# Performance work log

Hardware: AMD Instinct MI355X
Metric: run time of the kernel (lower is better)

Reference implementation:

```python
import jax, jax.numpy as jnp
import numpy as np

N = 2          # batch (upsample scale for sample i is i+1, shapes chosen so no crop occurs)
C = 512        # channels for both branches
TH = TW = 256  # target H,W taken from pts_feats[0]
IMG_SIZES = [128, 64, 32, 16, 8]  # 5-level FPN
BN_EPS = 1e-5


def setup_inputs() -> dict:
    key = jax.random.key(0)
    ks = jax.random.split(key, 24)
    inp = {}
    for l, s in enumerate(IMG_SIZES):
        inp[f'img_feat{l}'] = jax.random.normal(ks[l], (N, C, s, s), jnp.float32)
    inp['pts_feat0'] = jax.random.normal(ks[5], (N, C, TH, TW), jnp.float32)
    # 1x1 conv + BN params (eval-mode BN with running stats)
    inp['img_w'] = jax.random.normal(ks[6], (C, C), jnp.float32) * 0.02
    inp['img_b'] = jax.random.normal(ks[7], (C,), jnp.float32) * 0.02
    inp['img_gamma'] = jnp.ones((C,), jnp.float32)
    inp['img_beta'] = jnp.zeros((C,), jnp.float32)
    inp['img_mean'] = jnp.zeros((C,), jnp.float32)
    inp['img_var'] = jax.random.uniform(ks[8], (C,), jnp.float32, 0.5, 1.5)
    inp['pts_w'] = jax.random.normal(ks[9], (C, C), jnp.float32) * 0.02
    inp['pts_b'] = jax.random.normal(ks[10], (C,), jnp.float32) * 0.02
    inp['pts_gamma'] = jnp.ones((C,), jnp.float32)
    inp['pts_beta'] = jnp.zeros((C,), jnp.float32)
    inp['pts_mean'] = jnp.zeros((C,), jnp.float32)
    inp['pts_var'] = jax.random.uniform(ks[11], (C,), jnp.float32, 0.5, 1.5)
    return inp


def _obtain_mlvl(feats, th, tw):
    # Faithful to original: per-sample loop (scale_factor depends on batch index,
    # so each sample has a different static upsampled shape -> Python loop over N=2).
    n = feats[0].shape[0]
    outs = []
    for i in range(n):
        acc = None
        for lvl, f in enumerate(feats):
            x = f[i]  # [C, h, w]
            if lvl > 0:
                s = i + 1  # nearest upsample by batch-index+1 (as in source)
                x = jnp.repeat(jnp.repeat(x, s, axis=1), s, axis=2)
            dh = th - x.shape[1]
            dw = tw - x.shape[2]
            x = jnp.pad(x, ((0, 0), (dh // 2, dh - dh // 2), (dw // 2, dw - dw // 2)), mode='edge')
            acc = x if acc is None else acc + x
        outs.append(acc)
    return jnp.stack(outs, 0)  # [N, C, th, tw]


def _conv_bn_relu(x, w, b, gamma, beta, mean, var):
    # 1x1 conv == channel contraction, then eval-mode BN, then ReLU
    y = jnp.einsum('nchw,oc->nohw', x, w) + b[None, :, None, None]
    scale = gamma / jnp.sqrt(var + BN_EPS)
    y = (y - mean[None, :, None, None]) * scale[None, :, None, None] + beta[None, :, None, None]
    return jax.nn.relu(y)


def reference(img_feat0, img_feat1, img_feat2, img_feat3, img_feat4, pts_feat0,
              img_w, img_b, img_gamma, img_beta, img_mean, img_var,
              pts_w, pts_b, pts_gamma, pts_beta, pts_mean, pts_var):
    th, tw = pts_feat0.shape[2], pts_feat0.shape[3]
    pts_m = _obtain_mlvl([pts_feat0], th, tw)  # pts_levels=1
    pts_pre = _conv_bn_relu(pts_m, pts_w, pts_b, pts_gamma, pts_beta, pts_mean, pts_var)
    img_m = _obtain_mlvl([img_feat0, img_feat1, img_feat2, img_feat3, img_feat4], th, tw)
    img_pre = _conv_bn_relu(img_m, img_w, img_b, img_gamma, img_beta, img_mean, img_var)
    # dropout is identity in eval mode (deterministic reference)
    return jnp.concatenate((img_pre, pts_pre), axis=1)  # [N, 2C, th, tw]
```

## Files before the change

### kernel.cpp

```cpp
#include <hip/hip_runtime.h>

typedef unsigned short u16;
typedef __attribute__((ext_vector_type(8))) short s8frag;
typedef __attribute__((ext_vector_type(4))) float f32x4;

#define GLOAD16(gp, lp)                                                        \
  __builtin_amdgcn_global_load_lds(                                            \
      (const __attribute__((address_space(1))) void*)(gp),                     \
      (__attribute__((address_space(3))) void*)(lp), 16, 0, 0)

__device__ __forceinline__ u16 f2bf(float x) {
  unsigned int u = __float_as_uint(x);
  unsigned int r = (u + 0x7fffu + ((u >> 16) & 1u)) >> 16;
  return (u16)r;
}

__global__ __launch_bounds__(256) void prep_w(
    const float* __restrict__ wi, const float* __restrict__ bi,
    const float* __restrict__ gi, const float* __restrict__ bei,
    const float* __restrict__ mi, const float* __restrict__ vi,
    const float* __restrict__ wp, const float* __restrict__ bp,
    const float* __restrict__ gp, const float* __restrict__ bep,
    const float* __restrict__ mp, const float* __restrict__ vp,
    u16* __restrict__ wout_i, float* __restrict__ bias_i,
    u16* __restrict__ wout_p, float* __restrict__ bias_p) {
  int gidx = blockIdx.x * 256 + threadIdx.x;
  int branch = gidx >> 18;
  int idx = gidx & ((1 << 18) - 1);
  int o = idx >> 9, c = idx & 511;
  const float* w = branch ? wp : wi;
  const float* b = branch ? bp : bi;
  const float* g = branch ? gp : gi;
  const float* be = branch ? bep : bei;
  const float* mn = branch ? mp : mi;
  const float* vr = branch ? vp : vi;
  u16* wo = branch ? wout_p : wout_i;
  float* bo = branch ? bias_p : bias_i;
  float scale = g[o] * rsqrtf(vr[o] + 1e-5f);
  wo[idx] = f2bf(w[idx] * scale);
  if (c == 0) bo[o] = scale * (b[o] - mn[o]) + be[o];
}

__global__ __launch_bounds__(256) void build_b(
    const float* __restrict__ f0, const float* __restrict__ f1,
    const float* __restrict__ f2, const float* __restrict__ f3,
    const float* __restrict__ f4, const float* __restrict__ pts,
    u16* __restrict__ Bimg, u16* __restrict__ Bpts) {
  __shared__ float tile[64][65];
  int t = threadIdx.x;
  int wblk = blockIdx.x;
  int h = blockIdx.y;
  int z = blockIdx.z;
  bool is_img = z < 16;
  int zz = is_img ? z : z - 16;
  int n = zz >> 3;
  int cblk = zz & 7;
  int cbase = cblk * 64;

  if (is_img) {
    int wl = t & 63, w = wblk * 64 + wl;
    const float* feats[5] = {f0, f1, f2, f3, f4};
    const int S[5] = {128, 64, 32, 16, 8};
    int off[5];
#pragma unroll
    for (int l = 0; l < 5; ++l) {
      int s = S[l];
      int scale = (n == 1 && l > 0) ? 2 : 1;
      int u = s * scale, pad = (256 - u) >> 1;
      int ih = h - pad; ih = ih < 0 ? 0 : (ih > u - 1 ? u - 1 : ih); ih /= scale;
      int iw = w - pad; iw = iw < 0 ? 0 : (iw > u - 1 ? u - 1 : iw); iw /= scale;
      off[l] = ih * s + iw;
    }
    for (int cs = 0; cs < 16; ++cs) {
      int cl = cs * 4 + (t >> 6);
      int c = cbase + cl;
      float acc = 0.f;
#pragma unroll
      for (int l = 0; l < 5; ++l) {
        int s = S[l];
        acc += feats[l][(long)(n * 512 + c) * s * s + off[l]];
      }
      tile[cl][wl] = acc;
    }
  } else {
    int wq = t & 15;
    int cl0 = t >> 4;
#pragma unroll
    for (int j = 0; j < 4; ++j) {
      int cl = cl0 + j * 16;
      int c = cbase + cl;
      float4 v = *(const float4*)&pts[((long)(n * 512 + c) * 256 + h) * 256 +
                                      wblk * 64 + wq * 4];
      tile[cl][wq * 4 + 0] = v.x;
      tile[cl][wq * 4 + 1] = v.y;
      tile[cl][wq * 4 + 2] = v.z;
      tile[cl][wq * 4 + 3] = v.w;
    }
  }
  __syncthreads();

  u16* dst = is_img ? Bimg : Bpts;
  long hwb = (long)h * 256 + wblk * 64;
#pragma unroll
  for (int half = 0; half < 2; ++half) {
    int c0 = (t & 7) * 8;
    int wl2 = half * 32 + (t >> 3);
    u16 p[8];
#pragma unroll
    for (int j = 0; j < 8; ++j) p[j] = f2bf(tile[c0 + j][wl2]);
    long di = ((long)n * 65536 + hwb + wl2) * 512 + cbase + c0;
    *(uint4*)(dst + di) = *(const uint4*)p;
  }
}

__global__ __launch_bounds__(256, 2) void gemm_fused(
    const u16* __restrict__ Aimg, const u16* __restrict__ Apts,
    const u16* __restrict__ Bimg, const u16* __restrict__ Bpts,
    const float* __restrict__ biasImg, const float* __restrict__ biasPts,
    float* __restrict__ out) {
  int br = blockIdx.z;
  const u16* A = br ? Apts : Aimg;
  const u16* B = br ? Bpts : Bimg;
  const float* bias = br ? biasPts : biasImg;

  int s = blockIdx.x;
  int w = (s & 7) * 512 + (s >> 3);
  int rt = w & 3;
  int ct = w >> 2;
  int n = ct >> 9;
  int colbase = (ct & 511) * 128;
  const u16* Bn = B + ((long)n * 65536) * 512;

  __shared__ u16 As[2][128 * 64];
  __shared__ u16 Bs[2][128 * 64];

  int t = threadIdx.x;
  int wave = t >> 6, lane = t & 63;
  int wr = wave >> 1, wc = wave & 1;
  int lrow = lane & 15;
  int q = lane >> 4;

  f32x4 acc[4][4] = {};

#define STAGE_A(buf, kt_)                                                     \
  {                                                                           \
    int kk_ = (kt_) * 64;                                                     \
    _Pragma("unroll") for (int i = 0; i < 4; ++i) {                           \
      int slot = t + i * 256;                                                 \
      int row = slot >> 3, kp = slot & 7;                                     \
      GLOAD16(A + ((long)(rt * 128 + row) * 512 + kk_ + ((kp ^ (row & 7)) * 8)), \
              &As[buf][slot * 8]);                                            \
    }                                                                         \
  }
#define STAGE_B(buf, kt_)                                                     \
  {                                                                           \
    int kk_ = (kt_) * 64;                                                     \
    _Pragma("unroll") for (int i = 0; i < 4; ++i) {                           \
      int slot = t + i * 256;                                                 \
      int row = slot >> 3, kp = slot & 7;                                     \
      GLOAD16(Bn + ((long)(colbase + row) * 512 + kk_ + ((kp ^ (row & 7)) * 8)), \
              &Bs[buf][slot * 8]);                                            \
    }                                                                         \
  }

  STAGE_A(0, 0);
  STAGE_B(0, 0);
  asm volatile("s_waitcnt vmcnt(0)" ::: "memory");
  __builtin_amdgcn_s_barrier();

#pragma unroll 1
  for (int kt = 0; kt < 8; ++kt) {
    int cur = kt & 1;
    s8frag a[2][4], b[2][4];
#pragma unroll
    for (int sl = 0; sl < 2; ++sl) {
      int c = sl * 4 + q;
#pragma unroll
      for (int m = 0; m < 4; ++m) {
        int r = wr * 64 + m * 16 + lrow;
        a[sl][m] = *(const s8frag*)&As[cur][r * 64 + ((c ^ (r & 7)) * 8)];
      }
#pragma unroll
      for (int nn = 0; nn < 4; ++nn) {
        int r = wc * 64 + nn * 16 + lrow;
        b[sl][nn] = *(const s8frag*)&Bs[cur][r * 64 + ((c ^ (r & 7)) * 8)];
      }
    }
    if (kt < 7) {
      STAGE_A(cur ^ 1, kt + 1);
      STAGE_B(cur ^ 1, kt + 1);
    }
    __builtin_amdgcn_s_setprio(1);
#pragma unroll
    for (int sl = 0; sl < 2; ++sl)
#pragma unroll
      for (int m = 0; m < 4; ++m)
#pragma unroll
        for (int nn = 0; nn < 4; ++nn)
          acc[m][nn] = __builtin_amdgcn_mfma_f32_16x16x32_bf16(
              a[sl][m], b[sl][nn], acc[m][nn], 0, 0, 0);
    __builtin_amdgcn_s_setprio(0);
    if (kt < 7) {
      asm volatile("s_waitcnt vmcnt(0)" ::: "memory");
      __builtin_amdgcn_s_barrier();
    }
  }
#undef STAGE_A
#undef STAGE_B

  long outbase = ((long)n * 1024 + br * 512) * 65536;
#pragma unroll
  for (int m = 0; m < 4; ++m) {
    int o0 = rt * 128 + wr * 64 + m * 16 + q * 4;
#pragma unroll
    for (int nn = 0; nn < 4; ++nn) {
      int hw = colbase + wc * 64 + nn * 16 + lrow;
#pragma unroll
      for (int j = 0; j < 4; ++j) {
        int o = o0 + j;
        float v = acc[m][nn][j] + bias[o];
        v = v > 0.f ? v : 0.f;
        out[outbase + (long)o * 65536 + hw] = v;
      }
    }
  }
}

extern "C" void kernel_launch(void* const* d_in, const int* in_sizes, int n_in,
                              void* d_out, int out_size, void* d_ws,
                              size_t ws_size, hipStream_t stream) {
  (void)in_sizes; (void)n_in; (void)out_size; (void)ws_size;
  const float* f0 = (const float*)d_in[0];
  const float* f1 = (const float*)d_in[1];
  const float* f2 = (const float*)d_in[2];
  const float* f3 = (const float*)d_in[3];
  const float* f4 = (const float*)d_in[4];
  const float* pts = (const float*)d_in[5];
  const float* img_w = (const float*)d_in[6];
  const float* img_b = (const float*)d_in[7];
  const float* img_gamma = (const float*)d_in[8];
  const float* img_beta = (const float*)d_in[9];
  const float* img_mean = (const float*)d_in[10];
  const float* img_var = (const float*)d_in[11];
  const float* pts_w = (const float*)d_in[12];
  const float* pts_b = (const float*)d_in[13];
  const float* pts_gamma = (const float*)d_in[14];
  const float* pts_beta = (const float*)d_in[15];
  const float* pts_mean = (const float*)d_in[16];
  const float* pts_var = (const float*)d_in[17];

  char* ws = (char*)d_ws;
  u16* wA_img = (u16*)ws;
  u16* wA_pts = wA_img + 512 * 512;
  float* bias_img = (float*)(ws + (1u << 20));
  float* bias_pts = bias_img + 512;
  u16* Bimg = (u16*)(ws + (2u << 20));
  u16* Bpts = Bimg + (size_t)2 * 65536 * 512;

  prep_w<<<2048, 256, 0, stream>>>(img_w, img_b, img_gamma, img_beta, img_mean,
                                   img_var, pts_w, pts_b, pts_gamma, pts_beta,
                                   pts_mean, pts_var, wA_img, bias_img, wA_pts,
                                   bias_pts);
  build_b<<<dim3(4, 256, 32), 256, 0, stream>>>(f0, f1, f2, f3, f4, pts, Bimg,
                                                Bpts);
  gemm_fused<<<dim3(4096, 1, 2), 256, 0, stream>>>(
      wA_img, wA_pts, Bimg, Bpts, bias_img, bias_pts, (float*)d_out);
}
```

Baseline: 506.6 us.

## Make GEMM persistent over 8 column tiles with 4-stage K=32 pipeline

Each GEMM block now walks 8 consecutive 128-column tiles with a continuous software pipeline. It uses 4 LDS buffers of K=32 slices with a prefetch depth of 3 and partial vmcnt waits, and writes the epilogue after every 16 slices. The aim is to hide global-load latency across tile boundaries and remove the per-tile prologue and drain. The cost is 8x fewer blocks (1024 total), which can reduce occupancy and load balance, and epilogue stores now sit inside the main loop.

Measured after the change: 563.9 us. 1.11x slower.

```diff
diff --git a/kernel.cpp b/kernel.cpp
--- a/kernel.cpp
+++ b/kernel.cpp
@@ -123,16 +123,17 @@
   const u16* B = br ? Bpts : Bimg;
   const float* bias = br ? biasPts : biasImg;
 
-  int s = blockIdx.x;
-  int w = (s & 7) * 512 + (s >> 3);
+  int s0 = blockIdx.x;
+  int w = (s0 & 7) * 64 + (s0 >> 3);
   int rt = w & 3;
-  int ct = w >> 2;
-  int n = ct >> 9;
-  int colbase = (ct & 511) * 128;
+  int grp = w >> 2;
+  int n = (grp * 8) >> 9;
+  int cb0 = ((grp * 8) & 511) * 128;
   const u16* Bn = B + ((long)n * 65536) * 512;
-
-  __shared__ u16 As[2][128 * 64];
-  __shared__ u16 Bs[2][128 * 64];
+  long outbase = ((long)n * 1024 + br * 512) * 65536;
+
+  __shared__ u16 As[4][128 * 32];
+  __shared__ u16 Bs[4][128 * 32];
 
   int t = threadIdx.x;
   int wave = t >> 6, lane = t & 63;
@@ -142,88 +143,81 @@
 
   f32x4 acc[4][4] = {};
 
-#define STAGE_A(buf, kt_)                                                     \
+#define STAGE(s_)                                                             \
   {                                                                           \
-    int kk_ = (kt_) * 64;                                                     \
-    _Pragma("unroll") for (int i = 0; i < 4; ++i) {                           \
+    int buf_ = (s_) & 3;                                                      \
+    int kk_ = ((s_) & 15) * 32;                                               \
+    int cb_ = cb0 + ((s_) >> 4) * 128;                                        \
+    _Pragma("unroll") for (int i = 0; i < 2; ++i) {                           \
       int slot = t + i * 256;                                                 \
-      int row = slot >> 3, kp = slot & 7;                                     \
-      GLOAD16(A + ((long)(rt * 128 + row) * 512 + kk_ + ((kp ^ (row & 7)) * 8)), \
-              &As[buf][slot * 8]);                                            \
+      int row = slot >> 2, kp = slot & 3;                                     \
+      int sw = (row >> 1) & 3;                                                \
+      GLOAD16(A + ((long)(rt * 128 + row) * 512 + kk_ + ((kp ^ sw) * 8)),     \
+              &As[buf_][slot * 8]);                                           \
+      GLOAD16(Bn + ((long)(cb_ + row) * 512 + kk_ + ((kp ^ sw) * 8)),         \
+              &Bs[buf_][slot * 8]);                                           \
     }                                                                         \
   }
-#define STAGE_B(buf, kt_)                                                     \
-  {                                                                           \
-    int kk_ = (kt_) * 64;                                                     \
-    _Pragma("unroll") for (int i = 0; i < 4; ++i) {                           \
-      int slot = t + i * 256;                                                 \
-      int row = slot >> 3, kp = slot & 7;                                     \
-      GLOAD16(Bn + ((long)(colbase + row) * 512 + kk_ + ((kp ^ (row & 7)) * 8)), \
-              &Bs[buf][slot * 8]);                                            \
-    }                                                                         \
-  }
-
-  STAGE_A(0, 0);
-  STAGE_B(0, 0);
-  asm volatile("s_waitcnt vmcnt(0)" ::: "memory");
+
+  STAGE(0);
+  STAGE(1);
+  STAGE(2);
+  asm volatile("s_waitcnt vmcnt(8)" ::: "memory");
   __builtin_amdgcn_s_barrier();
 
 #pragma unroll 1
-  for (int kt = 0; kt < 8; ++kt) {
-    int cur = kt & 1;
-    s8frag a[2][4], b[2][4];
-#pragma unroll
-    for (int sl = 0; sl < 2; ++sl) {
-      int c = sl * 4 + q;
+  for (int s = 0; s < 128; ++s) {
+    int cur = s & 3;
+    s8frag a[4], b[4];
+#pragma unroll
+    for (int m = 0; m < 4; ++m) {
+      int r = wr * 64 + m * 16 + lrow;
+      a[m] = *(const s8frag*)&As[cur][r * 32 + ((q ^ ((r >> 1) & 3)) * 8)];
+    }
+#pragma unroll
+    for (int nn = 0; nn < 4; ++nn) {
+      int r = wc * 64 + nn * 16 + lrow;
+      b[nn] = *(const s8frag*)&Bs[cur][r * 32 + ((q ^ ((r >> 1) & 3)) * 8)];
+    }
+    if (s < 125) STAGE(s + 3);
+    __builtin_amdgcn_s_setprio(1);
+#pragma unroll
+    for (int m = 0; m < 4; ++m)
+#pragma unroll
+      for (int nn = 0; nn < 4; ++nn)
+        acc[m][nn] =
+            __builtin_amdgcn_mfma_f32_16x16x32_bf16(a[m], b[nn], acc[m][nn], 0, 0, 0);
+    __builtin_amdgcn_s_setprio(0);
+    if (s < 127) {
+      if (s < 125)
+        asm volatile("s_waitcnt vmcnt(8)" ::: "memory");
+      else if (s == 125)
+        asm volatile("s_waitcnt vmcnt(4)" ::: "memory");
+      else
+        asm volatile("s_waitcnt vmcnt(0)" ::: "memory");
+      __builtin_amdgcn_s_barrier();
+    }
+    if ((s & 15) == 15) {
+      int colbase = cb0 + (s >> 4) * 128;
 #pragma unroll
       for (int m = 0; m < 4; ++m) {
-        int r = wr * 64 + m * 16 + lrow;
-        a[sl][m] = *(const s8frag*)&As[cur][r * 64 + ((c ^ (r & 7)) * 8)];
+        int o0 = rt * 128 + wr * 64 + m * 16 + q * 4;
+#pragma unroll
+        for (int nn = 0; nn < 4; ++nn) {
+          int hw = colbase + wc * 64 + nn * 16 + lrow;
+#pragma unroll
+          for (int j = 0; j < 4; ++j) {
+            int o = o0 + j;
+            float v = acc[m][nn][j] + bias[o];
+            v = v > 0.f ? v : 0.f;
+            out[outbase + (long)o * 65536 + hw] = v;
+          }
+          acc[m][nn] = (f32x4){0.f, 0.f, 0.f, 0.f};
+        }
       }
-#pragma unroll
-      for (int nn = 0; nn < 4; ++nn) {
-        int r = wc * 64 + nn * 16 + lrow;
-        b[sl][nn] = *(const s8frag*)&Bs[cur][r * 64 + ((c ^ (r & 7)) * 8)];
-      }
-    }
-    if (kt < 7) {
-      STAGE_A(cur ^ 1, kt + 1);
-      STAGE_B(cur ^ 1, kt + 1);
-    }
-    __builtin_amdgcn_s_setprio(1);
-#pragma unroll
-    for (int sl = 0; sl < 2; ++sl)
-#pragma unroll
-      for (int m = 0; m < 4; ++m)
-#pragma unroll
-        for (int nn = 0; nn < 4; ++nn)
-          acc[m][nn] = __builtin_amdgcn_mfma_f32_16x16x32_bf16(
-              a[sl][m], b[sl][nn], acc[m][nn], 0, 0, 0);
-    __builtin_amdgcn_s_setprio(0);
-    if (kt < 7) {
-      asm volatile("s_waitcnt vmcnt(0)" ::: "memory");
-      __builtin_amdgcn_s_barrier();
-    }
-  }
-#undef STAGE_A
-#undef STAGE_B
-
-  long outbase = ((long)n * 1024 + br * 512) * 65536;
-#pragma unroll
-  for (int m = 0; m < 4; ++m) {
-    int o0 = rt * 128 + wr * 64 + m * 16 + q * 4;
-#pragma unroll
-    for (int nn = 0; nn < 4; ++nn) {
-      int hw = colbase + wc * 64 + nn * 16 + lrow;
-#pragma unroll
-      for (int j = 0; j < 4; ++j) {
-        int o = o0 + j;
-        float v = acc[m][nn][j] + bias[o];
-        v = v > 0.f ? v : 0.f;
-        out[outbase + (long)o * 65536 + hw] = v;
-      }
-    }
-  }
+    }
+  }
+#undef STAGE
 }
 
 extern "C" void kernel_launch(void* const* d_in, const int* in_sizes, int n_in,
@@ -263,6 +257,6 @@
                                    bias_pts);
   build_b<<<dim3(4, 256, 32), 256, 0, stream>>>(f0, f1, f2, f3, f4, pts, Bimg,
                                                 Bpts);
-  gemm_fused<<<dim3(4096, 1, 2), 256, 0, stream>>>(
+  gemm_fused<<<dim3(512, 1, 2), 256, 0, stream>>>(
       wA_img, wA_pts, Bimg, Bpts, bias_img, bias_pts, (float*)d_out);
 }
```
